# Optimization experiments

Hardware: AMD Instinct MI355X
Metric: run time of the kernel (lower is better)

Reference implementation:

```python
import jax, jax.numpy as jnp
import numpy as np

B, D, T = 16, 64, 256
BD = TD = H = 128
H2 = H // 2
NRES = 2


def setup_inputs() -> dict:
    key = jax.random.key(0)
    ks = jax.random.split(key, 24)
    r = lambda i, shape, s=0.05: jax.random.normal(ks[i], shape, jnp.float32) * s
    return {
        "branch_emb": jax.random.normal(ks[0], (B, D, BD), jnp.float32),
        "trunk_emb": jax.random.normal(ks[1], (B, T, TD), jnp.float32),
        "mask": jnp.ones((B, D), jnp.float32),
        "W_bil": r(2, (H, BD, TD)),
        "b_bil": r(3, (H,)),
        "W_br": r(4, (H, BD)), "b_br": r(5, (H,)),
        "W_tr": r(6, (H, TD)), "b_tr": r(7, (H,)),
        "g_fn": jnp.ones((H,), jnp.float32), "beta_fn": jnp.zeros((H,), jnp.float32),
        "res_w1": r(8, (NRES, H, H)), "res_b1": r(9, (NRES, H)),
        "res_w2": r(10, (NRES, H, H)), "res_b2": r(11, (NRES, H)),
        "res_g": jnp.ones((NRES, H), jnp.float32), "res_beta": jnp.zeros((NRES, H), jnp.float32),
        "pos_w1": r(12, (H2, H)), "pos_b1": r(13, (H2,)),
        "pos_w2": r(14, (1, H2)), "pos_b2": r(15, (1,)),
        "ex_w1": r(16, (H2, H)), "ex_b1": r(17, (H2,)),
        "ex_w2": r(18, (1, H2)), "ex_b2": r(19, (1,)),
    }


def _layer_norm(x, g, b, eps=1e-5):
    m = jnp.mean(x, axis=-1, keepdims=True)
    v = jnp.mean((x - m) ** 2, axis=-1, keepdims=True)
    return (x - m) * jax.lax.rsqrt(v + eps) * g + b


def reference(branch_emb, trunk_emb, mask, W_bil, b_bil, W_br, b_br, W_tr, b_tr,
              g_fn, beta_fn, res_w1, res_b1, res_w2, res_b2, res_g, res_beta,
              pos_w1, pos_b1, pos_w2, pos_b2, ex_w1, ex_b1, ex_w2, ex_b2):
    # Bilinear decomposition: never materialize the (B*D*T, dim) expanded inputs.
    # nn.Bilinear: out_h = x1 @ W[h] @ x2 + b[h]
    tmp = jnp.einsum('bdi,hij->bdhj', branch_emb, W_bil)          # (B,D,H,TD)
    fused = jnp.einsum('bdhj,btj->bdth', tmp, trunk_emb) + b_bil  # (B,D,T,H)
    fused = fused \
        + (branch_emb @ W_br.T + b_br)[:, :, None, :] \
        + (trunk_emb @ W_tr.T + b_tr)[:, None, :, :]
    fused = _layer_norm(fused, g_fn, beta_fn)
    for i in range(res_w1.shape[0]):
        h = jax.nn.gelu(fused @ res_w1[i].T + res_b1[i], approximate=False)
        h = h @ res_w2[i].T + res_b2[i]
        fused = _layer_norm(fused + h, res_g[i], res_beta[i])
    pos = jax.nn.gelu(fused @ pos_w1.T + pos_b1, approximate=False) @ pos_w2.T + pos_b2
    positions = jnp.clip(pos[..., 0], 0.0, 1.0)                   # (B,D,T)
    ex = jax.nn.gelu(fused @ ex_w1.T + ex_b1, approximate=False) @ ex_w2.T + ex_b2
    existence = jax.nn.sigmoid(ex[..., 0])                        # (B,D,T)
    m = mask[:, :, None]
    return positions * m, existence * m
```

## Files before the change

### kernel.cpp

```cpp
#include <hip/hip_runtime.h>
#include <hip/hip_bf16.h>

#define BDT_TOT 262144

typedef __attribute__((ext_vector_type(8))) short bf16x8;
typedef __attribute__((ext_vector_type(4))) float f32x4;

__device__ __forceinline__ unsigned short f2b(float f) {
  __hip_bfloat16 h = __float2bfloat16(f);
  return *reinterpret_cast<unsigned short*>(&h);
}
__device__ __forceinline__ float bu2f(unsigned u16) {
  union { unsigned u; float f; } c;
  c.u = u16 << 16;
  return c.f;
}
__device__ __forceinline__ float gelu_f(float x) {
  float x2 = x * x;
  float t = 1.5957691216057308f * x * fmaf(0.044715f, x2, 1.0f);
  return x * __builtin_amdgcn_rcpf(1.0f + __expf(-t));
}

__device__ __forceinline__ void gl16(const unsigned char* g, unsigned char* l) {
  __builtin_amdgcn_global_load_lds((const __attribute__((address_space(1))) unsigned int*)g,
                                   (__attribute__((address_space(3))) unsigned int*)l, 16, 0, 0);
}

__device__ __forceinline__ void stage_gl(const unsigned char* __restrict__ g, unsigned char* l,
                                         int w, int lane, int nkb) {
  const int per = nkb >> 2;
  const unsigned char* gp = g + ((w * per) << 10) + (lane << 4);
  unsigned char* lp = l + ((w * per) << 10);
  for (int i = 0; i < per; ++i) gl16(gp + (i << 10), lp + (i << 10));
}

__device__ __forceinline__ void stage_f32(unsigned char* dst, const float* __restrict__ src,
                                          int ld, int tid, int nch, int nthr) {
  for (int c = tid; c < nch; c += nthr) {
    int row = c >> 4, kc = c & 15;
    const float* s = src + row * ld + kc * 8;
    float4 u = *(const float4*)(s);
    float4 v = *(const float4*)(s + 4);
    union { unsigned short h[8]; uint4 q; } pk;
    pk.h[0] = f2b(u.x); pk.h[1] = f2b(u.y); pk.h[2] = f2b(u.z); pk.h[3] = f2b(u.w);
    pk.h[4] = f2b(v.x); pk.h[5] = f2b(v.y); pk.h[6] = f2b(v.z); pk.h[7] = f2b(v.w);
    *(uint4*)(dst + row * 256 + ((kc * 16) ^ ((row & 7) << 4))) = pk.q;
  }
}


__device__ __forceinline__ void gemm_tile(const unsigned char* Ar, const unsigned char* Br,
                                          int lane, int wm, int wn, f32x4 acc[4][2]) {
  const int lr = lane & 15, lk = lane >> 4;
#pragma unroll
  for (int ks = 0; ks < 4; ++ks) {
    const int kb = ks * 64 + lk * 16;
    bf16x8 a[4], bb[2];
#pragma unroll
    for (int mf = 0; mf < 4; ++mf) {
      int m = wm * 64 + mf * 16 + lr;
      a[mf] = *(const bf16x8*)(Ar + m * 256 + (kb ^ ((m & 7) << 4)));
    }
#pragma unroll
    for (int nf = 0; nf < 2; ++nf) {
      int n = wn * 32 + nf * 16 + lr;
      bb[nf] = *(const bf16x8*)(Br + n * 256 + (kb ^ ((n & 7) << 4)));
    }
#pragma unroll
    for (int mf = 0; mf < 4; ++mf)
#pragma unroll
      for (int nf = 0; nf < 2; ++nf)
        acc[mf][nf] = __builtin_amdgcn_mfma_f32_16x16x32_bf16(a[mf], bb[nf], acc[mf][nf], 0, 0, 0);
  }
}

__device__ __forceinline__ void gemm_tile64(const unsigned char* Ar, const unsigned char* Br,
                                            int lane, int wn, f32x4 acc[4][2]) {
  const int lr = lane & 15, lk = lane >> 4;
#pragma unroll
  for (int ks = 0; ks < 4; ++ks) {
    const int kb = ks * 64 + lk * 16;
    bf16x8 a[4], bb[2];
#pragma unroll
    for (int mf = 0; mf < 4; ++mf) {
      int m = mf * 16 + lr;
      a[mf] = *(const bf16x8*)(Ar + m * 256 + (kb ^ ((m & 7) << 4)));
    }
#pragma unroll
    for (int nf = 0; nf < 2; ++nf) {
      int n = wn * 32 + nf * 16 + lr;
      bb[nf] = *(const bf16x8*)(Br + n * 256 + (kb ^ ((n & 7) << 4)));
    }
#pragma unroll
    for (int mf = 0; mf < 4; ++mf)
#pragma unroll
      for (int nf = 0; nf < 2; ++nf)
        acc[mf][nf] = __builtin_amdgcn_mfma_f32_16x16x32_bf16(a[mf], bb[nf], acc[mf][nf], 0, 0, 0);
  }
}

__device__ __forceinline__ void zero_acc(f32x4 acc[4][2]) {
#pragma unroll
  for (int mf = 0; mf < 4; ++mf)
#pragma unroll
    for (int nf = 0; nf < 2; ++nf)
#pragma unroll
      for (int r = 0; r < 4; ++r) acc[mf][nf][r] = 0.0f;
}

__global__ __launch_bounds__(128) void rowlin_kernel(const float* __restrict__ in,
                                                     const float* __restrict__ W,
                                                     const float* __restrict__ b0,
                                                     const float* __restrict__ b1,
                                                     const float* __restrict__ b2,
                                                     float* __restrict__ out) {
  int r = blockIdx.x, h = threadIdx.x;
  __shared__ float xr[128];
  xr[h] = in[r * 128 + h];
  __syncthreads();
  const float* w = W + h * 128;
  float a = b0[h] + b1[h] + b2[h];
#pragma unroll 4
  for (int k = 0; k < 128; ++k) a = fmaf(xr[k], w[k], a);
  out[r * 128 + h] = a;
}

__global__ __launch_bounds__(256) void k_prep_cvt(
    const float* __restrict__ res_w1, const float* __restrict__ res_w2,
    const float* __restrict__ pos_w1, const float* __restrict__ ex_w1,
    const float* __restrict__ trunk,
    unsigned char* __restrict__ wTb, unsigned char* __restrict__ trunkb) {
  const int blk = blockIdx.x;
  const float* src; const float* src2 = nullptr; unsigned char* dst;
  if (blk == 0)      { src = res_w1;               dst = wTb; }
  else if (blk == 1) { src = res_w2;               dst = wTb + 32768; }
  else if (blk == 2) { src = res_w1 + 16384;       dst = wTb + 2 * 32768; }
  else if (blk == 3) { src = res_w2 + 16384;       dst = wTb + 3 * 32768; }
  else if (blk == 4) { src = pos_w1; src2 = ex_w1; dst = wTb + 4 * 32768; }
  else { src = trunk + (size_t)(blk - 5) * 16384; dst = trunkb + (size_t)(blk - 5) * 32768; }
  for (int c = threadIdx.x; c < 2048; c += 256) {
    const int row = c >> 4, kc = c & 15;
    const float* s = (src2 && row >= 64) ? (src2 + (row - 64) * 128 + kc * 8)
                                         : (src + row * 128 + kc * 8);
    float4 u = *(const float4*)s;
    float4 v = *(const float4*)(s + 4);
    union { unsigned short h[8]; uint4 q; } pk;
    pk.h[0]=f2b(u.x); pk.h[1]=f2b(u.y); pk.h[2]=f2b(u.z); pk.h[3]=f2b(u.w);
    pk.h[4]=f2b(v.x); pk.h[5]=f2b(v.y); pk.h[6]=f2b(v.z); pk.h[7]=f2b(v.w);
    *(uint4*)(dst + row * 256 + ((kc * 16) ^ ((row & 7) << 4))) = pk.q;
  }
}

struct SMemTmp {
  unsigned char A[32768];
  unsigned char Bt[32768];
};

__global__ __launch_bounds__(512, 2) void k_tmp(const float* __restrict__ be,
                                                const float* __restrict__ Wb,
                                                const float* __restrict__ W_tr,
                                                unsigned char* __restrict__ tmpb) {
  __shared__ SMemTmp sm;
  const int h = blockIdx.x >> 3, bd0 = (blockIdx.x & 7) << 7;
  const int tid = threadIdx.x, lane = tid & 63, w = tid >> 6, wm = w >> 2, wn = w & 3;
  const int lr = lane & 15, lk = lane >> 4;

  stage_f32(sm.A, be + bd0 * 128, 128, tid, 2048, 512);
  {
    const float* src = Wb + h * 16384;
    for (int it = tid; it < 4096; it += 512) {
      int i = it >> 5, j0 = (it & 31) * 4;
      float4 u = *(const float4*)(src + i * 128 + j0);
      float vv[4] = {u.x, u.y, u.z, u.w};
#pragma unroll
      for (int e = 0; e < 4; ++e) {
        int j = j0 + e;
        *(unsigned short*)(sm.Bt + j * 256 + ((2 * i) ^ ((j & 7) << 4))) = f2b(vv[e]);
      }
    }
  }
  __syncthreads();
  f32x4 acc[4][2];
  zero_acc(acc);
  gemm_tile(sm.A, sm.Bt, lane, wm, wn, acc);
  __syncthreads();
  float wtrv[2];
#pragma unroll
  for (int nf = 0; nf < 2; ++nf)
    wtrv[nf] = W_tr[h * 128 + wn * 32 + nf * 16 + lr];
#pragma unroll
  for (int mf = 0; mf < 4; ++mf)
#pragma unroll
    for (int nf = 0; nf < 2; ++nf)
#pragma unroll
      for (int r = 0; r < 4; ++r) {
        int row = wm * 64 + mf * 16 + lk * 4 + r;
        int col = wn * 32 + nf * 16 + lr;
        *(unsigned short*)(sm.A + row * 256 + col * 2) = f2b(acc[mf][nf][r] + wtrv[nf]);
      }
  __syncthreads();
  {
    int row = tid >> 2, part = tid & 3;
    const uint4* s = (const uint4*)(sm.A + row * 256 + part * 64);
    unsigned char* gt = tmpb + (size_t)(bd0 + row) * 32768 + h * 256;
    const int hx = (h & 7) << 4;
#pragma unroll
    for (int e = 0; e < 4; ++e)
      *(uint4*)(gt + ((part * 64 + e * 16) ^ hx)) = s[e];
  }
}

struct SMemMain {
  unsigned char A[16384];
  unsigned char Bm[32768];
  float ssum[64 * 4];
  float ssq[64 * 4];
  float part[2][64][2];
};

__device__ __forceinline__ void ln_store64(float (&x)[4][2][4], unsigned (&xp)[4][4],
                                           float* ssum, float* ssq,
                                           int lane, int wn,
                                           const float* __restrict__ g, const float* __restrict__ be,
                                           unsigned char* Adst,
                                           const unsigned char* stg_g, unsigned char* stg_l) {
  const int lr = lane & 15, lk = lane >> 4;
#pragma unroll
  for (int mf = 0; mf < 4; ++mf)
#pragma unroll
    for (int r = 0; r < 4; ++r) {
      float a = x[mf][0][r] + x[mf][1][r];
      float qq = x[mf][0][r] * x[mf][0][r] + x[mf][1][r] * x[mf][1][r];
#pragma unroll
      for (int m = 1; m < 16; m <<= 1) { a += __shfl_xor(a, m); qq += __shfl_xor(qq, m); }
      if (lr == 0) {
        int row = mf * 16 + lk * 4 + r;
        ssum[row * 4 + wn] = a;
        ssq[row * 4 + wn] = qq;
      }
    }
  __syncthreads();
  if (stg_g) stage_gl(stg_g, stg_l, wn, lane, 32);
  float gv[2], bv[2];
#pragma unroll
  for (int nf = 0; nf < 2; ++nf) {
    int col = wn * 32 + nf * 16 + lr;
    gv[nf] = g[col]; bv[nf] = be[col];
  }
#pragma unroll
  for (int mf = 0; mf < 4; ++mf)
#pragma unroll
    for (int r = 0; r < 4; ++r) {
      int row = mf * 16 + lk * 4 + r;
      float sum = ssum[row * 4 + 0] + ssum[row * 4 + 1] + ssum[row * 4 + 2] + ssum[row * 4 + 3];
      float sq  = ssq[row * 4 + 0] + ssq[row * 4 + 1] + ssq[row * 4 + 2] + ssq[row * 4 + 3];
      float mean = sum * 0.0078125f;
      float var  = sq * 0.0078125f - mean * mean;
      float rq = rsqrtf(var + 1e-5f);
      unsigned pk = 0;
#pragma unroll
      for (int nf = 0; nf < 2; ++nf) {
        int col = wn * 32 + nf * 16 + lr;
        float y = (x[mf][nf][r] - mean) * rq * gv[nf] + bv[nf];
        unsigned short us = f2b(y);
        pk |= ((unsigned)us) << (16 * nf);
        *(unsigned short*)(Adst + row * 256 + ((col * 2) ^ ((row & 7) << 4))) = us;
      }
      xp[mf][r] = pk;
    }
}

__global__ __launch_bounds__(256, 2) void k_main(
    const unsigned char* __restrict__ trunkb, const unsigned char* __restrict__ tmpb,
    const unsigned char* __restrict__ wTb,
    const float* __restrict__ br_all,
    const float* __restrict__ g_fn, const float* __restrict__ beta_fn,
    const float* __restrict__ res_b1, const float* __restrict__ res_b2,
    const float* __restrict__ res_g, const float* __restrict__ res_beta,
    const float* __restrict__ pos_b1, const float* __restrict__ pos_w2, const float* __restrict__ pos_b2,
    const float* __restrict__ ex_b1, const float* __restrict__ ex_w2, const float* __restrict__ ex_b2,
    const float* __restrict__ maskp, float* __restrict__ out) {
  __shared__ SMemMain sm;
  const int orig = blockIdx.x;
  const int gid = (orig & 7) * 512 + (orig >> 3);
  const int bd = gid >> 2, qt = gid & 3;
  const int b = bd >> 6, t0 = qt << 6;
  const int tid = threadIdx.x, lane = tid & 63, wn = tid >> 6;
  const int lr = lane & 15, lk = lane >> 4;

  stage_gl(trunkb + (size_t)(b * 256 + t0) * 256, sm.A, wn, lane, 16);
  stage_gl(tmpb + (size_t)bd * 32768, sm.Bm, wn, lane, 32);
  __syncthreads();
  f32x4 acc[4][2];
  zero_acc(acc);
  gemm_tile64(sm.A, sm.Bm, lane, wn, acc);

  unsigned xp[4][4];
  {
    float x[4][2][4];
#pragma unroll
    for (int nf = 0; nf < 2; ++nf) {
      int col = wn * 32 + nf * 16 + lr;
      float bb = br_all[bd * 128 + col];
#pragma unroll
      for (int mf = 0; mf < 4; ++mf)
#pragma unroll
        for (int r = 0; r < 4; ++r)
          x[mf][nf][r] = acc[mf][nf][r] + bb;
    }
    __syncthreads();
    ln_store64(x, xp, sm.ssum, sm.ssq, lane, wn, g_fn, beta_fn, sm.A, wTb, sm.Bm);
  }
  __syncthreads();

  for (int i = 0; i < 2; ++i) {
    zero_acc(acc);
    gemm_tile64(sm.A, sm.Bm, lane, wn, acc);
    __syncthreads();
    stage_gl(wTb + (size_t)(i * 2 + 1) * 32768, sm.Bm, wn, lane, 32);
#pragma unroll
    for (int nf = 0; nf < 2; ++nf) {
      int col = wn * 32 + nf * 16 + lr;
      float b1v = res_b1[i * 128 + col];
#pragma unroll
      for (int mf = 0; mf < 4; ++mf)
#pragma unroll
        for (int r = 0; r < 4; ++r) {
          int row = mf * 16 + lk * 4 + r;
          float hh = gelu_f(acc[mf][nf][r] + b1v);
          *(unsigned short*)(sm.A + row * 256 + ((col * 2) ^ ((row & 7) << 4))) = f2b(hh);
        }
    }
    __syncthreads();
    zero_acc(acc);
    gemm_tile64(sm.A, sm.Bm, lane, wn, acc);
    {
      float x[4][2][4];
#pragma unroll
      for (int nf = 0; nf < 2; ++nf) {
        int col = wn * 32 + nf * 16 + lr;
        float b2v = res_b2[i * 128 + col];
#pragma unroll
        for (int mf = 0; mf < 4; ++mf)
#pragma unroll
          for (int r = 0; r < 4; ++r)
            x[mf][nf][r] = bu2f((xp[mf][r] >> (16 * nf)) & 0xffffu) + acc[mf][nf][r] + b2v;
      }
      ln_store64(x, xp, sm.ssum, sm.ssq, lane, wn,
                 res_g + i * 128, res_beta + i * 128, sm.A,
                 wTb + (size_t)(i == 0 ? 2 : 4) * 32768, sm.Bm);
    }
    __syncthreads();
  }

  zero_acc(acc);
  gemm_tile64(sm.A, sm.Bm, lane, wn, acc);

  float s3[4][4];
#pragma unroll
  for (int mf = 0; mf < 4; ++mf)
#pragma unroll
    for (int r = 0; r < 4; ++r) s3[mf][r] = 0.0f;
#pragma unroll
  for (int nf = 0; nf < 2; ++nf) {
    int col = wn * 32 + nf * 16 + lr;
    float bias1 = (col < 64) ? pos_b1[col] : ex_b1[col - 64];
    float w2v = (col < 64) ? pos_w2[col] : ex_w2[col - 64];
#pragma unroll
    for (int mf = 0; mf < 4; ++mf)
#pragma unroll
      for (int r = 0; r < 4; ++r)
        s3[mf][r] += gelu_f(acc[mf][nf][r] + bias1) * w2v;
  }
#pragma unroll
  for (int mf = 0; mf < 4; ++mf)
#pragma unroll
    for (int r = 0; r < 4; ++r) {
      float a = s3[mf][r];
#pragma unroll
      for (int m = 1; m < 16; m <<= 1) a += __shfl_xor(a, m);
      s3[mf][r] = a;
    }
  if (lr == 0) {
#pragma unroll
    for (int mf = 0; mf < 4; ++mf)
#pragma unroll
      for (int r = 0; r < 4; ++r) {
        int row = mf * 16 + lk * 4 + r;
        sm.part[wn >> 1][row][wn & 1] = s3[mf][r];
      }
  }
  __syncthreads();
  if (tid < 128) {
    int row = tid >> 1, head = tid & 1;
    float v = sm.part[head][row][0] + sm.part[head][row][1];
    float mk = maskp[bd];
    int outr = bd * 256 + t0 + row;
    if (head == 0) {
      v += pos_b2[0];
      v = fminf(fmaxf(v, 0.0f), 1.0f);
      out[outr] = v * mk;
    } else {
      v += ex_b2[0];
      v = 1.0f / (1.0f + expf(-v));
      out[BDT_TOT + outr] = v * mk;
    }
  }
}

extern "C" void kernel_launch(void* const* d_in, const int* in_sizes, int n_in,
                              void* d_out, int out_size, void* d_ws, size_t ws_size,
                              hipStream_t stream) {
  const float* branch   = (const float*)d_in[0];
  const float* trunk    = (const float*)d_in[1];
  const float* mask     = (const float*)d_in[2];
  const float* W_bil    = (const float*)d_in[3];
  const float* b_bil    = (const float*)d_in[4];
  const float* W_br     = (const float*)d_in[5];
  const float* b_br     = (const float*)d_in[6];
  const float* W_tr     = (const float*)d_in[7];
  const float* b_tr     = (const float*)d_in[8];
  const float* g_fn     = (const float*)d_in[9];
  const float* beta_fn  = (const float*)d_in[10];
  const float* res_w1   = (const float*)d_in[11];
  const float* res_b1   = (const float*)d_in[12];
  const float* res_w2   = (const float*)d_in[13];
  const float* res_b2   = (const float*)d_in[14];
  const float* res_g    = (const float*)d_in[15];
  const float* res_beta = (const float*)d_in[16];
  const float* pos_w1   = (const float*)d_in[17];
  const float* pos_b1   = (const float*)d_in[18];
  const float* pos_w2   = (const float*)d_in[19];
  const float* pos_b2   = (const float*)d_in[20];
  const float* ex_w1    = (const float*)d_in[21];
  const float* ex_b1    = (const float*)d_in[22];
  const float* ex_w2    = (const float*)d_in[23];
  const float* ex_b2    = (const float*)d_in[24];
  float* out = (float*)d_out;

  unsigned char* wsb = (unsigned char*)d_ws;
  unsigned char* tmpb   = wsb;
  float* br_all         = (float*)(wsb + 33554432);
  unsigned char* wTb    = wsb + 34078720;
  unsigned char* trunkb = wsb + 34242560;

  hipLaunchKernelGGL(k_prep_cvt, dim3(37), dim3(256), 0, stream,
                     res_w1, res_w2, pos_w1, ex_w1, trunk, wTb, trunkb);
  hipLaunchKernelGGL(rowlin_kernel, dim3(1024), dim3(128), 0, stream,
                     branch, W_br, b_br, b_bil, b_tr, br_all);
  hipLaunchKernelGGL(k_tmp, dim3(1024), dim3(512), 0, stream, branch, W_bil, W_tr, tmpb);
  hipLaunchKernelGGL(k_main, dim3(4096), dim3(256), 0, stream,
                     trunkb, tmpb, wTb, br_all, g_fn, beta_fn,
                     res_b1, res_b2, res_g, res_beta,
                     pos_b1, pos_w2, pos_b2, ex_b1, ex_w2, ex_b2,
                     mask, out);
}
```

Measured before the change: 284.1 us.

## Split k_main 64-row tile across 8 waves instead of 4

k_main now launches 512 threads (8 waves) per block, arranged as 2 row-groups by 4 column-groups, so each wave computes a 32x32 output sub-tile instead of 64x32. The GEMM, LayerNorm, staging and head-reduction helpers are reworked for the new wave layout, and launch bounds change to (512,4). The aim is more waves per CU and fewer accumulator registers per thread, to hide latency in the chained small GEMMs. In exchange the B operand is read from LDS by twice as many waves, and barrier cost grows with the larger block.

```diff
diff --git a/kernel.cpp b/kernel.cpp
--- a/kernel.cpp
+++ b/kernel.cpp
@@ -26,9 +26,9 @@
                                    (__attribute__((address_space(3))) unsigned int*)l, 16, 0, 0);
 }
 
-__device__ __forceinline__ void stage_gl(const unsigned char* __restrict__ g, unsigned char* l,
-                                         int w, int lane, int nkb) {
-  const int per = nkb >> 2;
+__device__ __forceinline__ void stage_gl8(const unsigned char* __restrict__ g, unsigned char* l,
+                                          int w, int lane, int nkb) {
+  const int per = nkb >> 3;
   const unsigned char* gp = g + ((w * per) << 10) + (lane << 4);
   unsigned char* lp = l + ((w * per) << 10);
   for (int i = 0; i < per; ++i) gl16(gp + (i << 10), lp + (i << 10));
@@ -74,16 +74,16 @@
   }
 }
 
-__device__ __forceinline__ void gemm_tile64(const unsigned char* Ar, const unsigned char* Br,
-                                            int lane, int wn, f32x4 acc[4][2]) {
+__device__ __forceinline__ void gemm_tile32(const unsigned char* Ar, const unsigned char* Br,
+                                            int lane, int wm, int wn, f32x4 acc[2][2]) {
   const int lr = lane & 15, lk = lane >> 4;
 #pragma unroll
   for (int ks = 0; ks < 4; ++ks) {
     const int kb = ks * 64 + lk * 16;
-    bf16x8 a[4], bb[2];
-#pragma unroll
-    for (int mf = 0; mf < 4; ++mf) {
-      int m = mf * 16 + lr;
+    bf16x8 a[2], bb[2];
+#pragma unroll
+    for (int mf = 0; mf < 2; ++mf) {
+      int m = wm * 32 + mf * 16 + lr;
       a[mf] = *(const bf16x8*)(Ar + m * 256 + (kb ^ ((m & 7) << 4)));
     }
 #pragma unroll
@@ -92,16 +92,24 @@
       bb[nf] = *(const bf16x8*)(Br + n * 256 + (kb ^ ((n & 7) << 4)));
     }
 #pragma unroll
-    for (int mf = 0; mf < 4; ++mf)
+    for (int mf = 0; mf < 2; ++mf)
 #pragma unroll
       for (int nf = 0; nf < 2; ++nf)
         acc[mf][nf] = __builtin_amdgcn_mfma_f32_16x16x32_bf16(a[mf], bb[nf], acc[mf][nf], 0, 0, 0);
   }
 }
 
-__device__ __forceinline__ void zero_acc(f32x4 acc[4][2]) {
+__device__ __forceinline__ void zero_acc8(f32x4 acc[4][2]) {
 #pragma unroll
   for (int mf = 0; mf < 4; ++mf)
+#pragma unroll
+    for (int nf = 0; nf < 2; ++nf)
+#pragma unroll
+      for (int r = 0; r < 4; ++r) acc[mf][nf][r] = 0.0f;
+}
+__device__ __forceinline__ void zero_acc4(f32x4 acc[2][2]) {
+#pragma unroll
+  for (int mf = 0; mf < 2; ++mf)
 #pragma unroll
     for (int nf = 0; nf < 2; ++nf)
 #pragma unroll
@@ -181,7 +189,7 @@
   }
   __syncthreads();
   f32x4 acc[4][2];
-  zero_acc(acc);
+  zero_acc8(acc);
   gemm_tile(sm.A, sm.Bt, lane, wm, wn, acc);
   __syncthreads();
   float wtrv[2];
@@ -218,15 +226,15 @@
   float part[2][64][2];
 };
 
-__device__ __forceinline__ void ln_store64(float (&x)[4][2][4], unsigned (&xp)[4][4],
+__device__ __forceinline__ void ln_store32(float (&x)[2][2][4], unsigned (&xp)[2][4],
                                            float* ssum, float* ssq,
-                                           int lane, int wn,
+                                           int lane, int wm, int wn,
                                            const float* __restrict__ g, const float* __restrict__ be,
                                            unsigned char* Adst,
                                            const unsigned char* stg_g, unsigned char* stg_l) {
   const int lr = lane & 15, lk = lane >> 4;
 #pragma unroll
-  for (int mf = 0; mf < 4; ++mf)
+  for (int mf = 0; mf < 2; ++mf)
 #pragma unroll
     for (int r = 0; r < 4; ++r) {
       float a = x[mf][0][r] + x[mf][1][r];
@@ -234,13 +242,13 @@
 #pragma unroll
       for (int m = 1; m < 16; m <<= 1) { a += __shfl_xor(a, m); qq += __shfl_xor(qq, m); }
       if (lr == 0) {
-        int row = mf * 16 + lk * 4 + r;
+        int row = wm * 32 + mf * 16 + lk * 4 + r;
         ssum[row * 4 + wn] = a;
         ssq[row * 4 + wn] = qq;
       }
     }
   __syncthreads();
-  if (stg_g) stage_gl(stg_g, stg_l, wn, lane, 32);
+  if (stg_g) stage_gl8(stg_g, stg_l, wm * 4 + wn, lane, 32);
   float gv[2], bv[2];
 #pragma unroll
   for (int nf = 0; nf < 2; ++nf) {
@@ -248,10 +256,10 @@
     gv[nf] = g[col]; bv[nf] = be[col];
   }
 #pragma unroll
-  for (int mf = 0; mf < 4; ++mf)
+  for (int mf = 0; mf < 2; ++mf)
 #pragma unroll
     for (int r = 0; r < 4; ++r) {
-      int row = mf * 16 + lk * 4 + r;
+      int row = wm * 32 + mf * 16 + lk * 4 + r;
       float sum = ssum[row * 4 + 0] + ssum[row * 4 + 1] + ssum[row * 4 + 2] + ssum[row * 4 + 3];
       float sq  = ssq[row * 4 + 0] + ssq[row * 4 + 1] + ssq[row * 4 + 2] + ssq[row * 4 + 3];
       float mean = sum * 0.0078125f;
@@ -270,7 +278,7 @@
     }
 }
 
-__global__ __launch_bounds__(256, 2) void k_main(
+__global__ __launch_bounds__(512, 4) void k_main(
     const unsigned char* __restrict__ trunkb, const unsigned char* __restrict__ tmpb,
     const unsigned char* __restrict__ wTb,
     const float* __restrict__ br_all,
@@ -285,80 +293,81 @@
   const int gid = (orig & 7) * 512 + (orig >> 3);
   const int bd = gid >> 2, qt = gid & 3;
   const int b = bd >> 6, t0 = qt << 6;
-  const int tid = threadIdx.x, lane = tid & 63, wn = tid >> 6;
+  const int tid = threadIdx.x, lane = tid & 63;
+  const int w = tid >> 6, wm = w >> 2, wn = w & 3;
   const int lr = lane & 15, lk = lane >> 4;
 
-  stage_gl(trunkb + (size_t)(b * 256 + t0) * 256, sm.A, wn, lane, 16);
-  stage_gl(tmpb + (size_t)bd * 32768, sm.Bm, wn, lane, 32);
-  __syncthreads();
-  f32x4 acc[4][2];
-  zero_acc(acc);
-  gemm_tile64(sm.A, sm.Bm, lane, wn, acc);
-
-  unsigned xp[4][4];
+  stage_gl8(trunkb + (size_t)(b * 256 + t0) * 256, sm.A, w, lane, 16);
+  stage_gl8(tmpb + (size_t)bd * 32768, sm.Bm, w, lane, 32);
+  __syncthreads();
+  f32x4 acc[2][2];
+  zero_acc4(acc);
+  gemm_tile32(sm.A, sm.Bm, lane, wm, wn, acc);
+
+  unsigned xp[2][4];
   {
-    float x[4][2][4];
+    float x[2][2][4];
 #pragma unroll
     for (int nf = 0; nf < 2; ++nf) {
       int col = wn * 32 + nf * 16 + lr;
       float bb = br_all[bd * 128 + col];
 #pragma unroll
-      for (int mf = 0; mf < 4; ++mf)
+      for (int mf = 0; mf < 2; ++mf)
 #pragma unroll
         for (int r = 0; r < 4; ++r)
           x[mf][nf][r] = acc[mf][nf][r] + bb;
     }
     __syncthreads();
-    ln_store64(x, xp, sm.ssum, sm.ssq, lane, wn, g_fn, beta_fn, sm.A, wTb, sm.Bm);
+    ln_store32(x, xp, sm.ssum, sm.ssq, lane, wm, wn, g_fn, beta_fn, sm.A, wTb, sm.Bm);
   }
   __syncthreads();
 
   for (int i = 0; i < 2; ++i) {
-    zero_acc(acc);
-    gemm_tile64(sm.A, sm.Bm, lane, wn, acc);
+    zero_acc4(acc);
+    gemm_tile32(sm.A, sm.Bm, lane, wm, wn, acc);
     __syncthreads();
-    stage_gl(wTb + (size_t)(i * 2 + 1) * 32768, sm.Bm, wn, lane, 32);
+    stage_gl8(wTb + (size_t)(i * 2 + 1) * 32768, sm.Bm, w, lane, 32);
 #pragma unroll
     for (int nf = 0; nf < 2; ++nf) {
       int col = wn * 32 + nf * 16 + lr;
       float b1v = res_b1[i * 128 + col];
 #pragma unroll
-      for (int mf = 0; mf < 4; ++mf)
+      for (int mf = 0; mf < 2; ++mf)
 #pragma unroll
         for (int r = 0; r < 4; ++r) {
-          int row = mf * 16 + lk * 4 + r;
+          int row = wm * 32 + mf * 16 + lk * 4 + r;
           float hh = gelu_f(acc[mf][nf][r] + b1v);
           *(unsigned short*)(sm.A + row * 256 + ((col * 2) ^ ((row & 7) << 4))) = f2b(hh);
         }
     }
     __syncthreads();
-    zero_acc(acc);
-    gemm_tile64(sm.A, sm.Bm, lane, wn, acc);
+    zero_acc4(acc);
+    gemm_tile32(sm.A, sm.Bm, lane, wm, wn, acc);
     {
-      float x[4][2][4];
+      float x[2][2][4];
 #pragma unroll
       for (int nf = 0; nf < 2; ++nf) {
         int col = wn * 32 + nf * 16 + lr;
         float b2v = res_b2[i * 128 + col];
 #pragma unroll
-        for (int mf = 0; mf < 4; ++mf)
+        for (int mf = 0; mf < 2; ++mf)
 #pragma unroll
           for (int r = 0; r < 4; ++r)
             x[mf][nf][r] = bu2f((xp[mf][r] >> (16 * nf)) & 0xffffu) + acc[mf][nf][r] + b2v;
       }
-      ln_store64(x, xp, sm.ssum, sm.ssq, lane, wn,
+      ln_store32(x, xp, sm.ssum, sm.ssq, lane, wm, wn,
                  res_g + i * 128, res_beta + i * 128, sm.A,
                  wTb + (size_t)(i == 0 ? 2 : 4) * 32768, sm.Bm);
     }
     __syncthreads();
   }
 
-  zero_acc(acc);
-  gemm_tile64(sm.A, sm.Bm, lane, wn, acc);
-
-  float s3[4][4];
-#pragma unroll
-  for (int mf = 0; mf < 4; ++mf)
+  zero_acc4(acc);
+  gemm_tile32(sm.A, sm.Bm, lane, wm, wn, acc);
+
+  float s3[2][4];
+#pragma unroll
+  for (int mf = 0; mf < 2; ++mf)
 #pragma unroll
     for (int r = 0; r < 4; ++r) s3[mf][r] = 0.0f;
 #pragma unroll
@@ -367,13 +376,13 @@
     float bias1 = (col < 64) ? pos_b1[col] : ex_b1[col - 64];
     float w2v = (col < 64) ? pos_w2[col] : ex_w2[col - 64];
 #pragma unroll
-    for (int mf = 0; mf < 4; ++mf)
+    for (int mf = 0; mf < 2; ++mf)
 #pragma unroll
       for (int r = 0; r < 4; ++r)
         s3[mf][r] += gelu_f(acc[mf][nf][r] + bias1) * w2v;
   }
 #pragma unroll
-  for (int mf = 0; mf < 4; ++mf)
+  for (int mf = 0; mf < 2; ++mf)
 #pragma unroll
     for (int r = 0; r < 4; ++r) {
       float a = s3[mf][r];
@@ -383,10 +392,10 @@
     }
   if (lr == 0) {
 #pragma unroll
-    for (int mf = 0; mf < 4; ++mf)
+    for (int mf = 0; mf < 2; ++mf)
 #pragma unroll
       for (int r = 0; r < 4; ++r) {
-        int row = mf * 16 + lk * 4 + r;
+        int row = wm * 32 + mf * 16 + lk * 4 + r;
         sm.part[wn >> 1][row][wn & 1] = s3[mf][r];
       }
   }
@@ -449,7 +458,7 @@
   hipLaunchKernelGGL(rowlin_kernel, dim3(1024), dim3(128), 0, stream,
                      branch, W_br, b_br, b_bil, b_tr, br_all);
   hipLaunchKernelGGL(k_tmp, dim3(1024), dim3(512), 0, stream, branch, W_bil, W_tr, tmpb);
-  hipLaunchKernelGGL(k_main, dim3(4096), dim3(256), 0, stream,
+  hipLaunchKernelGGL(k_main, dim3(4096), dim3(512), 0, stream,
                      trunkb, tmpb, wTb, br_all, g_fn, beta_fn,
                      res_b1, res_b2, res_g, res_beta,
                      pos_b1, pos_w2, pos_b2, ex_b1, ex_w2, ex_b2,
```

Result: faster. 259.7 us (-8.6%).
